# Kernel optimization log

Measured on AMD Instinct MI355X. Metric: run time of the kernel, lower is better.

## Reference

```python
import jax, jax.numpy as jnp
import numpy as np


def _sage_layer(x, src, dst, w_self, w_neigh, b, n_dst):
    # sum-aggregate neighbor messages onto destination nodes
    agg = jax.ops.segment_sum(x[src], dst, num_segments=n_dst)  # [n_dst, d_in]
    # dst nodes are the first n_dst entries of the src frontier (standard layout)
    return x[:n_dst] @ w_self + agg @ w_neigh + b


def setup_inputs() -> dict:
    key = jax.random.key(0)
    ks = jax.random.split(key, 16)
    N0, N1, N2, N3 = 400000, 100000, 25000, 6250
    E0, E1, E2 = 1600000, 400000, 100000
    D, H, C = 256, 256, 47
    s = 1.0 / np.sqrt(D)
    return {
        "x": jax.random.normal(ks[0], (N0, D), dtype=jnp.float32),
        "src0": jax.random.randint(ks[1], (E0,), 0, N0),
        "dst0": jax.random.randint(ks[2], (E0,), 0, N1),
        "src1": jax.random.randint(ks[3], (E1,), 0, N1),
        "dst1": jax.random.randint(ks[4], (E1,), 0, N2),
        "src2": jax.random.randint(ks[5], (E2,), 0, N2),
        "dst2": jax.random.randint(ks[6], (E2,), 0, N3),
        "w_self0": jax.random.normal(ks[7], (D, H), dtype=jnp.float32) * s,
        "w_neigh0": jax.random.normal(ks[8], (D, H), dtype=jnp.float32) * s,
        "b0": jnp.zeros((H,), dtype=jnp.float32),
        "w_self1": jax.random.normal(ks[9], (H, H), dtype=jnp.float32) * s,
        "w_neigh1": jax.random.normal(ks[10], (H, H), dtype=jnp.float32) * s,
        "b1": jnp.zeros((H,), dtype=jnp.float32),
        "w_self2": jax.random.normal(ks[11], (H, C), dtype=jnp.float32) * s,
        "w_neigh2": jax.random.normal(ks[12], (H, C), dtype=jnp.float32) * s,
        "b2": jnp.zeros((C,), dtype=jnp.float32),
        "n_dst0": N1,
        "n_dst1": N2,
        "n_dst2": N3,
    }


def reference(x, src0, dst0, src1, dst1, src2, dst2,
              w_self0, w_neigh0, b0, w_self1, w_neigh1, b1,
              w_self2, w_neigh2, b2, n_dst0, n_dst1, n_dst2):
    h = _sage_layer(x, src0, dst0, w_self0, w_neigh0, b0, n_dst0)
    h = jax.nn.relu(h)  # dropout is identity in eval
    h = _sage_layer(h, src1, dst1, w_self1, w_neigh1, b1, n_dst1)
    h = jax.nn.relu(h)
    h = _sage_layer(h, src2, dst2, w_self2, w_neigh2, b2, n_dst2)
    return h
```

## Files before the change

kernel.cpp:

```cpp
#include <hip/hip_runtime.h>


#define DIM 256
#define CAP 64

typedef __attribute__((ext_vector_type(8))) short bf16x8;
typedef __attribute__((ext_vector_type(4))) float f32x4;

__device__ __forceinline__ short f2bf(float f) {
    union { float f; unsigned u; } v; v.f = f;
    unsigned r = v.u + 0x7FFF + ((v.u >> 16) & 1);
    return (short)(r >> 16);
}
__device__ __forceinline__ float bf2f(unsigned short h) {
    union { unsigned u; float f; } v; v.u = ((unsigned)h) << 16;
    return v.f;
}

#define GPTR(p) ((const __attribute__((address_space(1))) void*)(p))
#define LPTR(p) ((__attribute__((address_space(3))) void*)(p))

__global__ __launch_bounds__(256) void conv_x_kernel(
    const float* __restrict__ x, short* __restrict__ xb, int n4)
{
    int i = blockIdx.x * 256 + threadIdx.x;
    const int stride = gridDim.x * 256;
    for (; i < n4; i += stride) {
        const float4 v = ((const float4*)x)[i];
        short4 o;
        o.x = f2bf(v.x); o.y = f2bf(v.y); o.z = f2bf(v.z); o.w = f2bf(v.w);
        ((short4*)xb)[i] = o;
    }
}

__global__ __launch_bounds__(256) void bucket_all_kernel(
    const int* __restrict__ src0, const int* __restrict__ dst0, int E0,
    const int* __restrict__ src1, const int* __restrict__ dst1, int E1,
    const int* __restrict__ src2, const int* __restrict__ dst2, int E2,
    int* __restrict__ cur0, int* __restrict__ cur1, int* __restrict__ cur2,
    int* __restrict__ bk0, int* __restrict__ bk1, int* __restrict__ bk2)
{
    int e = blockIdx.x * 256 + threadIdx.x;
    const int* s; const int* d; int* cur; int* bk;
    if (e < E0)           { s = src0; d = dst0; cur = cur0; bk = bk0; }
    else if (e < E0 + E1) { e -= E0; s = src1; d = dst1; cur = cur1; bk = bk1; }
    else if (e < E0 + E1 + E2) { e -= E0 + E1; s = src2; d = dst2; cur = cur2; bk = bk2; }
    else return;
    const int dd = d[e];
    const int pos = atomicAdd(&cur[dd], 1);
    if (pos < CAP) bk[(size_t)dd * CAP + pos] = s[e];
}

template<bool F32IN>
__global__ __launch_bounds__(256) void agg_kernel(
    const void* __restrict__ Xv,
    const int* __restrict__ bucket,
    const int* __restrict__ cursor,
    short* __restrict__ agg,
    int n_dst)
{
    const int wave = (blockIdx.x << 2) + (threadIdx.x >> 6);
    if (wave >= n_dst) return;
    const int lane = threadIdx.x & 63;
    int deg = cursor[wave];
    if (deg > CAP) deg = CAP;
    const int* bk = bucket + (size_t)wave * CAP;

    float a0 = 0.f, a1 = 0.f, a2 = 0.f, a3 = 0.f;
    int j = 0;
    for (; j + 4 <= deg; j += 4) {
        const int s0 = bk[j], s1 = bk[j + 1], s2 = bk[j + 2], s3 = bk[j + 3];
        if (F32IN) {
            const float* X = (const float*)Xv;
            const float4 v0 = *(const float4*)(X + (size_t)s0 * DIM + lane * 4);
            const float4 v1 = *(const float4*)(X + (size_t)s1 * DIM + lane * 4);
            const float4 v2 = *(const float4*)(X + (size_t)s2 * DIM + lane * 4);
            const float4 v3 = *(const float4*)(X + (size_t)s3 * DIM + lane * 4);
            a0 += (v0.x + v1.x) + (v2.x + v3.x);
            a1 += (v0.y + v1.y) + (v2.y + v3.y);
            a2 += (v0.z + v1.z) + (v2.z + v3.z);
            a3 += (v0.w + v1.w) + (v2.w + v3.w);
        } else {
            const unsigned short* X = (const unsigned short*)Xv;
            const ushort4 u0 = *(const ushort4*)(X + (size_t)s0 * DIM + lane * 4);
            const ushort4 u1 = *(const ushort4*)(X + (size_t)s1 * DIM + lane * 4);
            const ushort4 u2 = *(const ushort4*)(X + (size_t)s2 * DIM + lane * 4);
            const ushort4 u3 = *(const ushort4*)(X + (size_t)s3 * DIM + lane * 4);
            a0 += (bf2f(u0.x) + bf2f(u1.x)) + (bf2f(u2.x) + bf2f(u3.x));
            a1 += (bf2f(u0.y) + bf2f(u1.y)) + (bf2f(u2.y) + bf2f(u3.y));
            a2 += (bf2f(u0.z) + bf2f(u1.z)) + (bf2f(u2.z) + bf2f(u3.z));
            a3 += (bf2f(u0.w) + bf2f(u1.w)) + (bf2f(u2.w) + bf2f(u3.w));
        }
    }
    for (; j < deg; ++j) {
        const int s0 = bk[j];
        if (F32IN) {
            const float* X = (const float*)Xv;
            const float4 v0 = *(const float4*)(X + (size_t)s0 * DIM + lane * 4);
            a0 += v0.x; a1 += v0.y; a2 += v0.z; a3 += v0.w;
        } else {
            const unsigned short* X = (const unsigned short*)Xv;
            const ushort4 u0 = *(const ushort4*)(X + (size_t)s0 * DIM + lane * 4);
            a0 += bf2f(u0.x); a1 += bf2f(u0.y); a2 += bf2f(u0.z); a3 += bf2f(u0.w);
        }
    }
    short4 o; o.x = f2bf(a0); o.y = f2bf(a1); o.z = f2bf(a2); o.w = f2bf(a3);
    *(short4*)(agg + (size_t)wave * DIM + lane * 4) = o;
}

__global__ __launch_bounds__(256) void wconv_kernel(
    const float* ws0, const float* wn0, const float* ws1, const float* wn1,
    const float* ws2, const float* wn2,
    short* t0, short* t1, short* t2, short* t3, short* t4, short* t5)
{
    const float* src; short* dst; int N, NP;
    switch (blockIdx.y) {
        case 0: src = ws0; dst = t0; N = 256; NP = 256; break;
        case 1: src = wn0; dst = t1; N = 256; NP = 256; break;
        case 2: src = ws1; dst = t2; N = 256; NP = 256; break;
        case 3: src = wn1; dst = t3; N = 256; NP = 256; break;
        case 4: src = ws2; dst = t4; N = 47;  NP = 128; break;
        default: src = wn2; dst = t5; N = 47; NP = 128; break;
    }
    int idx = blockIdx.x * 256 + threadIdx.x;
    if (idx >= NP * 256) return;
    int n = idx >> 8, k = idx & 255;
    float v = (n < N) ? src[(size_t)k * N + n] : 0.f;
    dst[(size_t)n * 256 + k] = f2bf(v);
}

template<bool A0F32, bool RELU, bool OUTF32>
__global__ __launch_bounds__(256) void mfma_gemm(
    const void* __restrict__ A0v,
    const short* __restrict__ A1,
    const short* __restrict__ B0,
    const short* __restrict__ B1,
    const float* __restrict__ bias,
    void* __restrict__ Cv,
    int M, int NV)
{
    __shared__ short As[128 * 32];
    __shared__ short Bs[128 * 32];

    const int t  = threadIdx.x;
    const int bm = blockIdx.x * 128;
    const int bn = blockIdx.y * 128;

    const int srow = t >> 2;
    const int scol = (t & 3) << 3;
    const int wv   = t >> 6;

    const int wm = (wv & 1) << 6;
    const int wn = (wv >> 1) << 6;
    const int lr = t & 15;
    const int lq = (t & 63) >> 4;

    f32x4 acc[4][4];
#pragma unroll
    for (int i = 0; i < 4; ++i)
#pragma unroll
        for (int j = 0; j < 4; ++j) {
            acc[i][j][0] = 0.f; acc[i][j][1] = 0.f; acc[i][j][2] = 0.f; acc[i][j][3] = 0.f;
        }

    for (int half = 0; half < 2; ++half) {
        const short* Bh = half ? B1 : B0;
        for (int kb = 0; kb < 256; kb += 32) {
            if (A0F32 && half == 0) {
                const float* A = (const float*)A0v;
#pragma unroll
                for (int i = 0; i < 2; ++i) {
                    int row = srow + i * 64;
                    int gm = bm + row; if (gm >= M) gm = M - 1;
                    const float* g = A + (size_t)gm * 256 + kb + scol;
                    const float4 u = *(const float4*)g;
                    const float4 w = *(const float4*)(g + 4);
                    bf16x8 pk;
                    pk[0] = f2bf(u.x); pk[1] = f2bf(u.y); pk[2] = f2bf(u.z); pk[3] = f2bf(u.w);
                    pk[4] = f2bf(w.x); pk[5] = f2bf(w.y); pk[6] = f2bf(w.z); pk[7] = f2bf(w.w);
                    *(bf16x8*)(As + row * 32 + scol) = pk;
                }
            } else {
                const short* Ah = (half == 0) ? (const short*)A0v : A1;
#pragma unroll
                for (int i = 0; i < 2; ++i) {
                    int row = srow + i * 64;
                    int gm = bm + row; if (gm >= M) gm = M - 1;
                    const short* g = Ah + (size_t)gm * 256 + kb + scol;
                    __builtin_amdgcn_global_load_lds(GPTR(g), LPTR(As + i * 2048 + wv * 512), 16, 0, 0);
                }
            }
#pragma unroll
            for (int i = 0; i < 2; ++i) {
                int row = srow + i * 64;
                const short* g = Bh + (size_t)(bn + row) * 256 + kb + scol;
                __builtin_amdgcn_global_load_lds(GPTR(g), LPTR(Bs + i * 2048 + wv * 512), 16, 0, 0);
            }
            __syncthreads();

            bf16x8 af[4], bfr[4];
#pragma unroll
            for (int i = 0; i < 4; ++i)
                af[i] = *(const bf16x8*)(As + (wm + i * 16 + lr) * 32 + lq * 8);
#pragma unroll
            for (int i = 0; i < 4; ++i)
                bfr[i] = *(const bf16x8*)(Bs + (wn + i * 16 + lr) * 32 + lq * 8);
#pragma unroll
            for (int mt = 0; mt < 4; ++mt)
#pragma unroll
                for (int nt = 0; nt < 4; ++nt)
                    acc[mt][nt] = __builtin_amdgcn_mfma_f32_16x16x32_bf16(af[mt], bfr[nt], acc[mt][nt], 0, 0, 0);
            __syncthreads();
        }
    }

#pragma unroll
    for (int nt = 0; nt < 4; ++nt) {
        const int gn = bn + wn + nt * 16 + lr;
        const float bv = bias[gn < NV ? gn : 0];
#pragma unroll
        for (int mt = 0; mt < 4; ++mt) {
            const f32x4 a = acc[mt][nt];
#pragma unroll
            for (int r = 0; r < 4; ++r) {
                const int gm = bm + wm + mt * 16 + lq * 4 + r;
                if (gm < M && gn < NV) {
                    float v = a[r] + bv;
                    if (RELU) v = fmaxf(v, 0.f);
                    if (OUTF32) ((float*)Cv)[(size_t)gm * NV + gn] = v;
                    else        ((short*)Cv)[(size_t)gm * NV + gn] = f2bf(v);
                }
            }
        }
    }
}

extern "C" void kernel_launch(void* const* d_in, const int* in_sizes, int n_in,
                              void* d_out, int out_size, void* d_ws, size_t ws_size,
                              hipStream_t stream) {
    (void)n_in; (void)out_size;

    const float* x    = (const float*)d_in[0];
    const int*   src0 = (const int*)d_in[1];
    const int*   dst0 = (const int*)d_in[2];
    const int*   src1 = (const int*)d_in[3];
    const int*   dst1 = (const int*)d_in[4];
    const int*   src2 = (const int*)d_in[5];
    const int*   dst2 = (const int*)d_in[6];
    const float* ws0  = (const float*)d_in[7];
    const float* wn0  = (const float*)d_in[8];
    const float* b0   = (const float*)d_in[9];
    const float* ws1  = (const float*)d_in[10];
    const float* wn1  = (const float*)d_in[11];
    const float* b1   = (const float*)d_in[12];
    const float* ws2  = (const float*)d_in[13];
    const float* wn2  = (const float*)d_in[14];
    const float* b2   = (const float*)d_in[15];

    const int E0 = in_sizes[1];
    const int E1 = in_sizes[3];
    const int E2 = in_sizes[5];
    const int N0 = 400000, N1 = 100000, N2 = 25000, N3 = 6250;

    char* p = (char*)d_ws;
    auto alloc = [&](size_t bytes) { char* r = p; p += (bytes + 255) & ~(size_t)255; return r; };
    short* h0   = (short*)alloc((size_t)N1 * DIM * 2);
    short* h1   = (short*)alloc((size_t)N2 * DIM * 2);
    short* agg  = (short*)alloc((size_t)N1 * DIM * 2);
    int*   bk0  = (int*)alloc((size_t)N1 * CAP * 4);
    int*   bk1  = (int*)alloc((size_t)N2 * CAP * 4);
    int*   bk2  = (int*)alloc((size_t)N3 * CAP * 4);
    int*   curs = (int*)alloc((size_t)(N1 + N2 + N3) * 4);
    short* wt0s = (short*)alloc(256 * 256 * 2);
    short* wt0n = (short*)alloc(256 * 256 * 2);
    short* wt1s = (short*)alloc(256 * 256 * 2);
    short* wt1n = (short*)alloc(256 * 256 * 2);
    short* wt2s = (short*)alloc(128 * 256 * 2);
    short* wt2n = (short*)alloc(128 * 256 * 2);
    const size_t base_bytes = (size_t)(p - (char*)d_ws);
    const size_t xbf_bytes  = (size_t)N0 * DIM * 2;
    const bool   use_xbf    = (base_bytes + xbf_bytes) <= ws_size;
    short* x_bf = (short*)alloc(xbf_bytes);

    int* cur0 = curs, *cur1 = curs + N1, *cur2 = curs + N1 + N2;
    const int Etot = E0 + E1 + E2;

    if (use_xbf)
        conv_x_kernel<<<8192, 256, 0, stream>>>(x, x_bf, N0 * DIM / 4);
    wconv_kernel<<<dim3(256, 6), 256, 0, stream>>>(ws0, wn0, ws1, wn1, ws2, wn2,
                                                   wt0s, wt0n, wt1s, wt1n, wt2s, wt2n);
    hipMemsetAsync(curs, 0, (size_t)(N1 + N2 + N3) * 4, stream);
    bucket_all_kernel<<<(Etot + 255) / 256, 256, 0, stream>>>(
        src0, dst0, E0, src1, dst1, E1, src2, dst2, E2,
        cur0, cur1, cur2, bk0, bk1, bk2);

    if (use_xbf) {
        agg_kernel<false><<<(N1 + 3) / 4, 256, 0, stream>>>(x_bf, bk0, cur0, agg, N1);
        mfma_gemm<false, true, false><<<dim3((N1 + 127) / 128, 2), 256, 0, stream>>>(
            x_bf, agg, wt0s, wt0n, b0, h0, N1, 256);
    } else {
        agg_kernel<true><<<(N1 + 3) / 4, 256, 0, stream>>>(x, bk0, cur0, agg, N1);
        mfma_gemm<true, true, false><<<dim3((N1 + 127) / 128, 2), 256, 0, stream>>>(
            x, agg, wt0s, wt0n, b0, h0, N1, 256);
    }
    agg_kernel<false><<<(N2 + 3) / 4, 256, 0, stream>>>(h0, bk1, cur1, agg, N2);
    mfma_gemm<false, true, false><<<dim3((N2 + 127) / 128, 2), 256, 0, stream>>>(
        h0, agg, wt1s, wt1n, b1, h1, N2, 256);
    agg_kernel<false><<<(N3 + 3) / 4, 256, 0, stream>>>(h1, bk2, cur2, agg, N3);
    mfma_gemm<false, false, true><<<dim3((N3 + 127) / 128, 1), 256, 0, stream>>>(
        h1, agg, wt2s, wt2n, b2, d_out, N3, 47);
}
```

Baseline: 1.041 ms.

## Merge prep kernels, widen bf16 gather unroll, process K=64 per GEMM sync

Folds the x-to-bf16 conversion and weight transpose/convert into one launch, removing a kernel launch. The bf16 aggregation loop now issues eight independent row gathers per iteration to raise memory-level parallelism. The GEMM stages two 32-wide K slices into doubled LDS buffers before each barrier, halving the number of sync points at the cost of more shared memory per block. LAYER template parameters are added only to separate instantiations.

```diff
diff --git a/kernel.cpp b/kernel.cpp
--- a/kernel.cpp
+++ b/kernel.cpp
@@ -20,20 +20,39 @@
 #define GPTR(p) ((const __attribute__((address_space(1))) void*)(p))
 #define LPTR(p) ((__attribute__((address_space(3))) void*)(p))
 
-__global__ __launch_bounds__(256) void conv_x_kernel(
-    const float* __restrict__ x, short* __restrict__ xb, int n4)
+__global__ __launch_bounds__(256) void prep_kernel(
+    const float* __restrict__ x, short* __restrict__ xb, int n4, int cb,
+    const float* __restrict__ ws0, const float* __restrict__ wn0,
+    const float* __restrict__ ws1, const float* __restrict__ wn1,
+    const float* __restrict__ ws2, const float* __restrict__ wn2,
+    short* t0, short* t1, short* t2, short* t3, short* t4, short* t5)
 {
-    int i = blockIdx.x * 256 + threadIdx.x;
-    const int stride = gridDim.x * 256;
-    for (; i < n4; i += stride) {
-        const float4 v = ((const float4*)x)[i];
-        short4 o;
-        o.x = f2bf(v.x); o.y = f2bf(v.y); o.z = f2bf(v.z); o.w = f2bf(v.w);
-        ((short4*)xb)[i] = o;
-    }
-}
-
-__global__ __launch_bounds__(256) void bucket_all_kernel(
+    if ((int)blockIdx.x < cb) {
+        int i = blockIdx.x * 256 + threadIdx.x;
+        const int stride = cb * 256;
+        for (; i < n4; i += stride) {
+            const float4 v = ((const float4*)x)[i];
+            short4 o;
+            o.x = f2bf(v.x); o.y = f2bf(v.y); o.z = f2bf(v.z); o.w = f2bf(v.w);
+            ((short4*)xb)[i] = o;
+        }
+        return;
+    }
+    int idx = (blockIdx.x - cb) * 256 + threadIdx.x;
+    const float* src; short* dst; int N, base;
+    if (idx < 65536)       { src = ws0; dst = t0; N = 256; base = 0; }
+    else if (idx < 131072) { src = wn0; dst = t1; N = 256; base = 65536; }
+    else if (idx < 196608) { src = ws1; dst = t2; N = 256; base = 131072; }
+    else if (idx < 262144) { src = wn1; dst = t3; N = 256; base = 196608; }
+    else if (idx < 294912) { src = ws2; dst = t4; N = 47;  base = 262144; }
+    else if (idx < 327680) { src = wn2; dst = t5; N = 47;  base = 294912; }
+    else return;
+    const int l = idx - base;
+    const int n = l >> 8, k = l & 255;
+    dst[(size_t)n * 256 + k] = f2bf(n < N ? src[(size_t)k * N + n] : 0.f);
+}
+
+__global__ __launch_bounds__(256) void bucket_edges(
     const int* __restrict__ src0, const int* __restrict__ dst0, int E0,
     const int* __restrict__ src1, const int* __restrict__ dst1, int E1,
     const int* __restrict__ src2, const int* __restrict__ dst2, int E2,
@@ -51,7 +70,7 @@
     if (pos < CAP) bk[(size_t)dd * CAP + pos] = s[e];
 }
 
-template<bool F32IN>
+template<int LAYER, bool F32IN>
 __global__ __launch_bounds__(256) void agg_kernel(
     const void* __restrict__ Xv,
     const int* __restrict__ bucket,
@@ -68,10 +87,10 @@
 
     float a0 = 0.f, a1 = 0.f, a2 = 0.f, a3 = 0.f;
     int j = 0;
-    for (; j + 4 <= deg; j += 4) {
-        const int s0 = bk[j], s1 = bk[j + 1], s2 = bk[j + 2], s3 = bk[j + 3];
-        if (F32IN) {
-            const float* X = (const float*)Xv;
+    if (F32IN) {
+        const float* X = (const float*)Xv;
+        for (; j + 4 <= deg; j += 4) {
+            const int s0 = bk[j], s1 = bk[j + 1], s2 = bk[j + 2], s3 = bk[j + 3];
             const float4 v0 = *(const float4*)(X + (size_t)s0 * DIM + lane * 4);
             const float4 v1 = *(const float4*)(X + (size_t)s1 * DIM + lane * 4);
             const float4 v2 = *(const float4*)(X + (size_t)s2 * DIM + lane * 4);
@@ -80,27 +99,34 @@
             a1 += (v0.y + v1.y) + (v2.y + v3.y);
             a2 += (v0.z + v1.z) + (v2.z + v3.z);
             a3 += (v0.w + v1.w) + (v2.w + v3.w);
-        } else {
-            const unsigned short* X = (const unsigned short*)Xv;
-            const ushort4 u0 = *(const ushort4*)(X + (size_t)s0 * DIM + lane * 4);
-            const ushort4 u1 = *(const ushort4*)(X + (size_t)s1 * DIM + lane * 4);
-            const ushort4 u2 = *(const ushort4*)(X + (size_t)s2 * DIM + lane * 4);
-            const ushort4 u3 = *(const ushort4*)(X + (size_t)s3 * DIM + lane * 4);
-            a0 += (bf2f(u0.x) + bf2f(u1.x)) + (bf2f(u2.x) + bf2f(u3.x));
-            a1 += (bf2f(u0.y) + bf2f(u1.y)) + (bf2f(u2.y) + bf2f(u3.y));
-            a2 += (bf2f(u0.z) + bf2f(u1.z)) + (bf2f(u2.z) + bf2f(u3.z));
-            a3 += (bf2f(u0.w) + bf2f(u1.w)) + (bf2f(u2.w) + bf2f(u3.w));
-        }
-    }
-    for (; j < deg; ++j) {
-        const int s0 = bk[j];
-        if (F32IN) {
-            const float* X = (const float*)Xv;
-            const float4 v0 = *(const float4*)(X + (size_t)s0 * DIM + lane * 4);
+        }
+        for (; j < deg; ++j) {
+            const float4 v0 = *(const float4*)(X + (size_t)bk[j] * DIM + lane * 4);
             a0 += v0.x; a1 += v0.y; a2 += v0.z; a3 += v0.w;
-        } else {
-            const unsigned short* X = (const unsigned short*)Xv;
-            const ushort4 u0 = *(const ushort4*)(X + (size_t)s0 * DIM + lane * 4);
+        }
+    } else {
+        const unsigned short* X = (const unsigned short*)Xv;
+        for (; j + 8 <= deg; j += 8) {
+            ushort4 u[8];
+#pragma unroll
+            for (int q = 0; q < 8; ++q)
+                u[q] = *(const ushort4*)(X + (size_t)bk[j + q] * DIM + lane * 4);
+#pragma unroll
+            for (int q = 0; q < 8; ++q) {
+                a0 += bf2f(u[q].x); a1 += bf2f(u[q].y);
+                a2 += bf2f(u[q].z); a3 += bf2f(u[q].w);
+            }
+        }
+        for (; j + 2 <= deg; j += 2) {
+            const ushort4 u0 = *(const ushort4*)(X + (size_t)bk[j] * DIM + lane * 4);
+            const ushort4 u1 = *(const ushort4*)(X + (size_t)bk[j + 1] * DIM + lane * 4);
+            a0 += bf2f(u0.x) + bf2f(u1.x);
+            a1 += bf2f(u0.y) + bf2f(u1.y);
+            a2 += bf2f(u0.z) + bf2f(u1.z);
+            a3 += bf2f(u0.w) + bf2f(u1.w);
+        }
+        if (j < deg) {
+            const ushort4 u0 = *(const ushort4*)(X + (size_t)bk[j] * DIM + lane * 4);
             a0 += bf2f(u0.x); a1 += bf2f(u0.y); a2 += bf2f(u0.z); a3 += bf2f(u0.w);
         }
     }
@@ -108,28 +134,7 @@
     *(short4*)(agg + (size_t)wave * DIM + lane * 4) = o;
 }
 
-__global__ __launch_bounds__(256) void wconv_kernel(
-    const float* ws0, const float* wn0, const float* ws1, const float* wn1,
-    const float* ws2, const float* wn2,
-    short* t0, short* t1, short* t2, short* t3, short* t4, short* t5)
-{
-    const float* src; short* dst; int N, NP;
-    switch (blockIdx.y) {
-        case 0: src = ws0; dst = t0; N = 256; NP = 256; break;
-        case 1: src = wn0; dst = t1; N = 256; NP = 256; break;
-        case 2: src = ws1; dst = t2; N = 256; NP = 256; break;
-        case 3: src = wn1; dst = t3; N = 256; NP = 256; break;
-        case 4: src = ws2; dst = t4; N = 47;  NP = 128; break;
-        default: src = wn2; dst = t5; N = 47; NP = 128; break;
-    }
-    int idx = blockIdx.x * 256 + threadIdx.x;
-    if (idx >= NP * 256) return;
-    int n = idx >> 8, k = idx & 255;
-    float v = (n < N) ? src[(size_t)k * N + n] : 0.f;
-    dst[(size_t)n * 256 + k] = f2bf(v);
-}
-
-template<bool A0F32, bool RELU, bool OUTF32>
+template<int LAYER, bool A0F32, bool RELU, bool OUTF32>
 __global__ __launch_bounds__(256) void mfma_gemm(
     const void* __restrict__ A0v,
     const short* __restrict__ A1,
@@ -139,8 +144,8 @@
     void* __restrict__ Cv,
     int M, int NV)
 {
-    __shared__ short As[128 * 32];
-    __shared__ short Bs[128 * 32];
+    __shared__ short As[2][128 * 32];
+    __shared__ short Bs[2][128 * 32];
 
     const int t  = threadIdx.x;
     const int bm = blockIdx.x * 128;
@@ -155,6 +160,9 @@
     const int lr = t & 15;
     const int lq = (t & 63) >> 4;
 
+    int gmA = bm + srow;        if (gmA >= M) gmA = M - 1;
+    int gmA2 = bm + srow + 64;  if (gmA2 >= M) gmA2 = M - 1;
+
     f32x4 acc[4][4];
 #pragma unroll
     for (int i = 0; i < 4; ++i)
@@ -165,51 +173,53 @@
 
     for (int half = 0; half < 2; ++half) {
         const short* Bh = half ? B1 : B0;
-        for (int kb = 0; kb < 256; kb += 32) {
-            if (A0F32 && half == 0) {
-                const float* A = (const float*)A0v;
-#pragma unroll
-                for (int i = 0; i < 2; ++i) {
-                    int row = srow + i * 64;
-                    int gm = bm + row; if (gm >= M) gm = M - 1;
-                    const float* g = A + (size_t)gm * 256 + kb + scol;
-                    const float4 u = *(const float4*)g;
-                    const float4 w = *(const float4*)(g + 4);
-                    bf16x8 pk;
-                    pk[0] = f2bf(u.x); pk[1] = f2bf(u.y); pk[2] = f2bf(u.z); pk[3] = f2bf(u.w);
-                    pk[4] = f2bf(w.x); pk[5] = f2bf(w.y); pk[6] = f2bf(w.z); pk[7] = f2bf(w.w);
-                    *(bf16x8*)(As + row * 32 + scol) = pk;
+        for (int kb = 0; kb < 256; kb += 64) {
+#pragma unroll
+            for (int sub = 0; sub < 2; ++sub) {
+                const int kk = kb + sub * 32;
+                if (A0F32 && half == 0) {
+                    const float* A = (const float*)A0v;
+#pragma unroll
+                    for (int i = 0; i < 2; ++i) {
+                        const int gm = i ? gmA2 : gmA;
+                        const int row = srow + i * 64;
+                        const float* g = A + (size_t)gm * 256 + kk + scol;
+                        const float4 u = *(const float4*)g;
+                        const float4 w = *(const float4*)(g + 4);
+                        bf16x8 pk;
+                        pk[0] = f2bf(u.x); pk[1] = f2bf(u.y); pk[2] = f2bf(u.z); pk[3] = f2bf(u.w);
+                        pk[4] = f2bf(w.x); pk[5] = f2bf(w.y); pk[6] = f2bf(w.z); pk[7] = f2bf(w.w);
+                        *(bf16x8*)(&As[sub][row * 32 + scol]) = pk;
+                    }
+                } else {
+                    const short* Ah = half ? A1 : (const short*)A0v;
+                    __builtin_amdgcn_global_load_lds(GPTR(Ah + (size_t)gmA  * 256 + kk + scol),
+                                                     LPTR(&As[sub][0]    + wv * 512), 16, 0, 0);
+                    __builtin_amdgcn_global_load_lds(GPTR(Ah + (size_t)gmA2 * 256 + kk + scol),
+                                                     LPTR(&As[sub][2048] + wv * 512), 16, 0, 0);
                 }
-            } else {
-                const short* Ah = (half == 0) ? (const short*)A0v : A1;
-#pragma unroll
-                for (int i = 0; i < 2; ++i) {
-                    int row = srow + i * 64;
-                    int gm = bm + row; if (gm >= M) gm = M - 1;
-                    const short* g = Ah + (size_t)gm * 256 + kb + scol;
-                    __builtin_amdgcn_global_load_lds(GPTR(g), LPTR(As + i * 2048 + wv * 512), 16, 0, 0);
-                }
-            }
-#pragma unroll
-            for (int i = 0; i < 2; ++i) {
-                int row = srow + i * 64;
-                const short* g = Bh + (size_t)(bn + row) * 256 + kb + scol;
-                __builtin_amdgcn_global_load_lds(GPTR(g), LPTR(Bs + i * 2048 + wv * 512), 16, 0, 0);
+                __builtin_amdgcn_global_load_lds(GPTR(Bh + (size_t)(bn + srow)      * 256 + kk + scol),
+                                                 LPTR(&Bs[sub][0]    + wv * 512), 16, 0, 0);
+                __builtin_amdgcn_global_load_lds(GPTR(Bh + (size_t)(bn + srow + 64) * 256 + kk + scol),
+                                                 LPTR(&Bs[sub][2048] + wv * 512), 16, 0, 0);
             }
             __syncthreads();
 
-            bf16x8 af[4], bfr[4];
-#pragma unroll
-            for (int i = 0; i < 4; ++i)
-                af[i] = *(const bf16x8*)(As + (wm + i * 16 + lr) * 32 + lq * 8);
-#pragma unroll
-            for (int i = 0; i < 4; ++i)
-                bfr[i] = *(const bf16x8*)(Bs + (wn + i * 16 + lr) * 32 + lq * 8);
-#pragma unroll
-            for (int mt = 0; mt < 4; ++mt)
-#pragma unroll
-                for (int nt = 0; nt < 4; ++nt)
-                    acc[mt][nt] = __builtin_amdgcn_mfma_f32_16x16x32_bf16(af[mt], bfr[nt], acc[mt][nt], 0, 0, 0);
+#pragma unroll
+            for (int sub = 0; sub < 2; ++sub) {
+                bf16x8 af[4], bfr[4];
+#pragma unroll
+                for (int i = 0; i < 4; ++i)
+                    af[i] = *(const bf16x8*)(&As[sub][(wm + i * 16 + lr) * 32 + lq * 8]);
+#pragma unroll
+                for (int i = 0; i < 4; ++i)
+                    bfr[i] = *(const bf16x8*)(&Bs[sub][(wn + i * 16 + lr) * 32 + lq * 8]);
+#pragma unroll
+                for (int mt = 0; mt < 4; ++mt)
+#pragma unroll
+                    for (int nt = 0; nt < 4; ++nt)
+                        acc[mt][nt] = __builtin_amdgcn_mfma_f32_16x16x32_bf16(af[mt], bfr[nt], acc[mt][nt], 0, 0, 0);
+            }
             __syncthreads();
         }
     }
@@ -284,29 +294,29 @@
 
     int* cur0 = curs, *cur1 = curs + N1, *cur2 = curs + N1 + N2;
     const int Etot = E0 + E1 + E2;
-
-    if (use_xbf)
-        conv_x_kernel<<<8192, 256, 0, stream>>>(x, x_bf, N0 * DIM / 4);
-    wconv_kernel<<<dim3(256, 6), 256, 0, stream>>>(ws0, wn0, ws1, wn1, ws2, wn2,
-                                                   wt0s, wt0n, wt1s, wt1n, wt2s, wt2n);
+    const int conv_blocks = use_xbf ? 8192 : 0;
+
+    prep_kernel<<<conv_blocks + 1280, 256, 0, stream>>>(
+        x, x_bf, N0 * DIM / 4, conv_blocks,
+        ws0, wn0, ws1, wn1, ws2, wn2, wt0s, wt0n, wt1s, wt1n, wt2s, wt2n);
     hipMemsetAsync(curs, 0, (size_t)(N1 + N2 + N3) * 4, stream);
-    bucket_all_kernel<<<(Etot + 255) / 256, 256, 0, stream>>>(
+    bucket_edges<<<(Etot + 255) / 256, 256, 0, stream>>>(
         src0, dst0, E0, src1, dst1, E1, src2, dst2, E2,
         cur0, cur1, cur2, bk0, bk1, bk2);
 
     if (use_xbf) {
-        agg_kernel<false><<<(N1 + 3) / 4, 256, 0, stream>>>(x_bf, bk0, cur0, agg, N1);
-        mfma_gemm<false, true, false><<<dim3((N1 + 127) / 128, 2), 256, 0, stream>>>(
+        agg_kernel<0, false><<<(N1 + 3) / 4, 256, 0, stream>>>(x_bf, bk0, cur0, agg, N1);
+        mfma_gemm<0, false, true, false><<<dim3((N1 + 127) / 128, 2), 256, 0, stream>>>(
             x_bf, agg, wt0s, wt0n, b0, h0, N1, 256);
     } else {
-        agg_kernel<true><<<(N1 + 3) / 4, 256, 0, stream>>>(x, bk0, cur0, agg, N1);
-        mfma_gemm<true, true, false><<<dim3((N1 + 127) / 128, 2), 256, 0, stream>>>(
+        agg_kernel<0, true><<<(N1 + 3) / 4, 256, 0, stream>>>(x, bk0, cur0, agg, N1);
+        mfma_gemm<0, true, true, false><<<dim3((N1 + 127) / 128, 2), 256, 0, stream>>>(
             x, agg, wt0s, wt0n, b0, h0, N1, 256);
     }
-    agg_kernel<false><<<(N2 + 3) / 4, 256, 0, stream>>>(h0, bk1, cur1, agg, N2);
-    mfma_gemm<false, true, false><<<dim3((N2 + 127) / 128, 2), 256, 0, stream>>>(
+    agg_kernel<1, false><<<(N2 + 3) / 4, 256, 0, stream>>>(h0, bk1, cur1, agg, N2);
+    mfma_gemm<1, false, true, false><<<dim3((N2 + 127) / 128, 2), 256, 0, stream>>>(
         h0, agg, wt1s, wt1n, b1, h1, N2, 256);
-    agg_kernel<false><<<(N3 + 3) / 4, 256, 0, stream>>>(h1, bk2, cur2, agg, N3);
-    mfma_gemm<false, false, true><<<dim3((N3 + 127) / 128, 1), 256, 0, stream>>>(
+    agg_kernel<2, false><<<(N3 + 3) / 4, 256, 0, stream>>>(h1, bk2, cur2, agg, N3);
+    mfma_gemm<2, false, false, true><<<dim3((N3 + 127) / 128, 1), 256, 0, stream>>>(
         h1, agg, wt2s, wt2n, b2, d_out, N3, 47);
 }
```

Result: no change. 1.049 ms (+0.8%).
